# Kernel tuning notes

Measured on AMD Instinct MI355X. Metric: run time of the kernel, lower is better.

## Reference

```python
import jax, jax.numpy as jnp
import numpy as np
from jax import lax

B, S, F, H = 64, 512, 512, 1024
P = 0.5        # fixed power exponent (p_required_learn=False)
EPS = 1e-3     # epsilon default in forward


def setup_inputs() -> dict:
    key = jax.random.key(0)
    ks = jax.random.split(key, 10)
    x = jax.random.normal(ks[0], (B, S, F), dtype=jnp.float32)
    # monotonically nondecreasing times per batch row (arange fill)
    time_sequence = jnp.arange(B * S * 1, dtype=jnp.float32).reshape(B, S, 1)
    std = 1.0 / np.sqrt(H)
    def w(k, shape):
        return jax.random.normal(k, shape, dtype=jnp.float32) * std
    return {
        "x": x,
        "time_sequence": time_sequence,
        "U_r": w(ks[1], (F, H)), "W_r": w(ks[2], (H, H)),
        "b_r": jax.random.uniform(ks[3], (H,), jnp.float32, -std, std),
        "U_c": w(ks[4], (F, H)), "W_c": w(ks[5], (H, H)),
        "b_c": jax.random.uniform(ks[6], (H,), jnp.float32, -std, std),
        "U_o": w(ks[7], (F, H)), "W_o": w(ks[8], (H, H)),
        "b_o": jax.random.uniform(ks[9], (H,), jnp.float32, -std, std),
    }


def _plstm(x, time_sequence, U_r, W_r, b_r, U_c, W_c, b_c, U_o, W_o, b_o):
    b, s, f = x.shape
    h = W_r.shape[0]
    # input projections are h-independent: precompute for all timesteps
    xr = jnp.einsum('bsf,fh->bsh', x, U_r) + b_r  # [B,S,H]
    xc = jnp.einsum('bsf,fh->bsh', x, U_c) + b_c
    xo = jnp.einsum('bsf,fh->bsh', x, U_o) + b_o

    def step(carry, inp):
        h_t, c_t, k_t = carry
        xr_t, xc_t, xo_t, t = inp          # [B,H],[B,H],[B,H],[B,1]
        r_t = jax.nn.sigmoid(xr_t + h_t @ W_r)
        k_t = r_t * t + (1.0 - r_t) * k_t
        c_tilde = jnp.tanh(xc_t + h_t @ W_c)
        d = t - k_t
        f_t = ((d + 1.0) / (d + EPS)) ** (-P)
        c_t = f_t * c_t + (1.0 - f_t) * c_tilde
        o_t = jax.nn.sigmoid(xo_t + h_t @ W_o)
        h_t = o_t * jnp.tanh(c_t)
        return (h_t, c_t, k_t), h_t

    z = jnp.zeros((b, h), dtype=x.dtype)
    xs = (xr.transpose(1, 0, 2), xc.transpose(1, 0, 2), xo.transpose(1, 0, 2),
          time_sequence.transpose(1, 0, 2))
    (h_T, c_T, k_T), hs = lax.scan(step, (z, z, z), xs)
    hidden_seq = hs.transpose(1, 0, 2)  # [B,S,H]
    return hidden_seq, (h_T, c_T, k_T)


def reference(x, time_sequence, U_r, W_r, b_r, U_c, W_c, b_c, U_o, W_o, b_o):
    return _plstm(x, time_sequence, U_r, W_r, b_r, U_c, W_c, b_c, U_o, W_o, b_o)
```

## Files before the change

### kernel.cpp

```cpp
#include <hip/hip_runtime.h>
#include <hip/hip_fp16.h>
#include <cstdint>
#include <cstddef>

#define B_   64
#define S_   512
#define F_   512
#define H_   1024
#define KTOT 1536
#define EPS_ 1e-3f
#define NBLK 256
#define NTHR 512

typedef _Float16 f16x8 __attribute__((ext_vector_type(8)));
typedef float    f32x4 __attribute__((ext_vector_type(4)));

#define WS_CNT_OFF  0
#define WS_HBUF_OFF 4096
#define WS_WT_OFF   (1024*1024)

#define MFMA16(A,Bf,C) __builtin_amdgcn_mfma_f32_16x16x32_f16(A, Bf, C, 0, 0, 0)

__global__ void prep_weights(const float* __restrict__ Wr, const float* __restrict__ Wc,
                             const float* __restrict__ Wo, const float* __restrict__ Ur,
                             const float* __restrict__ Uc, const float* __restrict__ Uo,
                             _Float16* __restrict__ Wt) {
    int b  = blockIdx.x;
    int g  = b >> 6;
    int j0 = (b & 63) << 4;
    const float* W = (g == 0) ? Wr : (g == 1) ? Wc : Wo;
    const float* U = (g == 0) ? Ur : (g == 1) ? Uc : Uo;
    int jj = threadIdx.x & 15;
    int kk = threadIdx.x >> 4;
    for (int k0 = 0; k0 < KTOT; k0 += 16) {
        int k = k0 + kk;
        float v = (k < H_) ? W[(size_t)k * H_ + j0 + jj]
                           : U[(size_t)(k - H_) * H_ + j0 + jj];
        Wt[(size_t)(g * H_ + j0 + jj) * KTOT + k] = (_Float16)v;
    }
}

__global__ __launch_bounds__(NTHR, 2)
void plstm_cnt(const float* __restrict__ x,
               const float* __restrict__ ts,
               const float* __restrict__ br,
               const float* __restrict__ bc,
               const float* __restrict__ bo,
               const _Float16* __restrict__ Wt,
               _Float16* __restrict__ hbuf,
               unsigned* __restrict__ cnt,
               float* __restrict__ out) {
    __shared__ float    red[8 * 768];
    __shared__ _Float16 hlog[64 * 256];

    const int tid = threadIdx.x;
    const int bid = blockIdx.x;
    const int grp = bid >> 5;
    const int cg  = bid & 31;
    const int r0  = grp << 3;
    const int c0  = cg << 5;

    const int lane = tid & 63;
    const int w    = tid >> 6;
    const int arow = r0 + (lane & 7);
    const int kblk = lane >> 4;
    const int jcol = lane & 15;

    f16x8 bfh[3][2][4], bfx[3][2][2];
    #pragma unroll
    for (int g3 = 0; g3 < 3; ++g3)
        #pragma unroll
        for (int ct = 0; ct < 2; ++ct) {
            const _Float16* base = Wt + (size_t)(g3 * H_ + c0 + ct * 16 + jcol) * KTOT;
            #pragma unroll
            for (int sub = 0; sub < 4; ++sub)
                bfh[g3][ct][sub] = *(const f16x8*)(base + w * 128 + sub * 32 + kblk * 8);
            #pragma unroll
            for (int sub = 0; sub < 2; ++sub)
                bfx[g3][ct][sub] = *(const f16x8*)(base + H_ + w * 64 + sub * 32 + kblk * 8);
        }

    const int erow = tid >> 5;
    const int ecol = tid & 31;
    const int gb   = r0 + (erow & 7);
    const int gh   = c0 + ecol;
    float biasr = 0.f, biasc = 0.f, biaso = 0.f;
    if (tid < 256) { biasr = br[gh]; biasc = bc[gh]; biaso = bo[gh]; }
    float cst = 0.f, kst = 0.f, hval = 0.f;

    const unsigned* const cp = cnt + grp * 32;

    f32x4 xn0, xn1, xn2, xn3; float tvn = 0.f;
    {
        const float* xp = x + (size_t)arow * S_ * F_ + w * 64 + kblk * 8;
        xn0 = *(const f32x4*)xp;        xn1 = *(const f32x4*)(xp + 4);
        xn2 = *(const f32x4*)(xp + 32); xn3 = *(const f32x4*)(xp + 36);
        if (tid < 256) tvn = ts[(size_t)gb * S_];
        else if (w < 4) tvn = 0.f;
    }
    f16x8 xf0, xf1;
    #pragma unroll
    for (int r = 0; r < 4; ++r) { xf0[r] = (_Float16)xn0[r]; xf0[4 + r] = (_Float16)xn1[r]; }
    #pragma unroll
    for (int r = 0; r < 4; ++r) { xf1[r] = (_Float16)xn2[r]; xf1[4 + r] = (_Float16)xn3[r]; }
    float tv = tvn;

    for (int t = 0; t < S_; ++t) {
        f32x4 acc[3][2] = {};
        #pragma unroll
        for (int g3 = 0; g3 < 3; ++g3)
            #pragma unroll
            for (int ct = 0; ct < 2; ++ct) {
                acc[g3][ct] = MFMA16(xf0, bfx[g3][ct][0], acc[g3][ct]);
                acc[g3][ct] = MFMA16(xf1, bfx[g3][ct][1], acc[g3][ct]);
            }

        if (t > 0) {
            const unsigned tgt = 32u * (unsigned)t;
            unsigned c;
            for (unsigned it = 0; it < (1u << 17); ++it) {
                asm volatile("global_load_dword %0, %1, off sc0 sc1\n\t"
                             "s_waitcnt vmcnt(0)"
                             : "=v"(c) : "v"(cp) : "memory");
                if (c >= tgt) break;
            }
        }
        __builtin_amdgcn_sched_barrier(0);

        const _Float16* hb = hbuf + (size_t)(t % 3) * B_ * H_
                                  + (size_t)arow * H_ + w * 128 + kblk * 8;
        f16x8 hfr[4];
        #pragma unroll
        for (int s = 0; s < 4; ++s)
            asm volatile("global_load_dwordx4 %0, %1, off sc0 sc1"
                         : "=v"(hfr[s]) : "v"(hb + s * 32));
        asm volatile("s_waitcnt vmcnt(0)" ::: "memory");
        __builtin_amdgcn_sched_barrier(0);

        if (t + 1 < S_) {
            const float* xp = x + ((size_t)arow * S_ + (t + 1)) * F_ + w * 64 + kblk * 8;
            xn0 = *(const f32x4*)xp;        xn1 = *(const f32x4*)(xp + 4);
            xn2 = *(const f32x4*)(xp + 32); xn3 = *(const f32x4*)(xp + 36);
            if (tid < 256) tvn = ts[(size_t)gb * S_ + t + 1];
        }

        #pragma unroll
        for (int s = 0; s < 4; ++s)
            #pragma unroll
            for (int g3 = 0; g3 < 3; ++g3) {
                acc[g3][0] = MFMA16(hfr[s], bfh[g3][0][s], acc[g3][0]);
                acc[g3][1] = MFMA16(hfr[s], bfh[g3][1][s], acc[g3][1]);
            }

        if (lane < 32) {
            float* rw = red + w * 768;
            const int crow = (lane >> 4) << 2;
            const int ccol = lane & 15;
            #pragma unroll
            for (int i = 0; i < 4; ++i) {
                const int rr = (crow + i) * 32 + ccol;
                rw[rr]              = acc[0][0][i];  rw[rr + 16]         = acc[0][1][i];
                rw[256 + rr]        = acc[1][0][i];  rw[256 + rr + 16]   = acc[1][1][i];
                rw[512 + rr]        = acc[2][0][i];  rw[512 + rr + 16]   = acc[2][1][i];
            }
        }
        __syncthreads();

        float pr = biasr, pc = biasc, po = biaso;
        if (tid < 256) {
            #pragma unroll
            for (int ww = 0; ww < 8; ++ww) {
                pr += red[ww * 768 + tid];
                pc += red[ww * 768 + 256 + tid];
                po += red[ww * 768 + 512 + tid];
            }
        }

        if (tid < 256) {
            const float r = 1.f / (1.f + __expf(-pr));
            kst = r * tv + (1.f - r) * kst;
            const float e2 = __expf(2.f * pc);
            const float ctil = (e2 - 1.f) / (e2 + 1.f);
            const float d = tv - kst;
            const float f = __fsqrt_rn((d + EPS_) / (d + 1.f));
            cst = f * cst + (1.f - f) * ctil;
            const float o = 1.f / (1.f + __expf(-po));
            const float e2c = __expf(2.f * cst);
            hval = o * ((e2c - 1.f) / (e2c + 1.f));

            if (t + 1 < S_) {
                union { _Float16 hf; unsigned short us; } cv; cv.hf = (_Float16)hval;
                unsigned short* hp = (unsigned short*)(hbuf
                    + (size_t)((t + 1) % 3) * B_ * H_ + (size_t)gb * H_ + gh);
                unsigned uv = cv.us;
                asm volatile("global_store_short %0, %1, off sc0 sc1"
                             :: "v"(hp), "v"(uv) : "memory");
            }
            hlog[(t & 63) * 256 + tid] = (_Float16)hval;
        }

        asm volatile("s_waitcnt vmcnt(0)" ::: "memory");
        __syncthreads();
        if (tid == 0 && t + 1 < S_)
            __hip_atomic_fetch_add((unsigned*)cp, 1u,
                                   __ATOMIC_RELAXED, __HIP_MEMORY_SCOPE_AGENT);

        if (tid >= 256 && (t & 31) == 0 && t) {
            const int tbase = t - 32;
            #pragma unroll
            for (int p = 0; p < 4; ++p) {
                const int m  = p * 256 + (tid - 256);
                const int dt = m >> 5;
                const int c  = m & 31;
                f16x8 v = *(const f16x8*)(hlog + ((tbase + dt) & 63) * 256 + c * 8);
                float* op = out + ((size_t)(r0 + (c >> 2)) * S_ + tbase + dt) * H_
                                + c0 + (c & 3) * 8;
                f32x4 o0, o1;
                #pragma unroll
                for (int r2 = 0; r2 < 4; ++r2) { o0[r2] = (float)v[r2]; o1[r2] = (float)v[4 + r2]; }
                *(f32x4*)op = o0;
                *(f32x4*)(op + 4) = o1;
            }
        }

        if (t + 1 < S_) {
            #pragma unroll
            for (int r2 = 0; r2 < 4; ++r2) { xf0[r2] = (_Float16)xn0[r2]; xf0[4 + r2] = (_Float16)xn1[r2]; }
            #pragma unroll
            for (int r2 = 0; r2 < 4; ++r2) { xf1[r2] = (_Float16)xn2[r2]; xf1[4 + r2] = (_Float16)xn3[r2]; }
            tv = tvn;
        }
    }

    __syncthreads();
    {
        const int tbase = S_ - 32;
        #pragma unroll
        for (int p = 0; p < 2; ++p) {
            const int m  = p * 512 + tid;
            const int dt = m >> 5;
            const int c  = m & 31;
            f16x8 v = *(const f16x8*)(hlog + ((tbase + dt) & 63) * 256 + c * 8);
            float* op = out + ((size_t)(r0 + (c >> 2)) * S_ + tbase + dt) * H_
                            + c0 + (c & 3) * 8;
            f32x4 o0, o1;
            #pragma unroll
            for (int r2 = 0; r2 < 4; ++r2) { o0[r2] = (float)v[r2]; o1[r2] = (float)v[4 + r2]; }
            *(f32x4*)op = o0;
            *(f32x4*)(op + 4) = o1;
        }
    }
    if (tid < 256) {
        const size_t BSH = (size_t)B_ * S_ * H_;
        out[BSH +                       (size_t)gb * H_ + gh] = hval;
        out[BSH + (size_t)B_ * H_ +     (size_t)gb * H_ + gh] = cst;
        out[BSH + 2 * (size_t)B_ * H_ + (size_t)gb * H_ + gh] = kst;
    }
}

extern "C" void kernel_launch(void* const* d_in, const int* in_sizes, int n_in,
                              void* d_out, int out_size, void* d_ws, size_t ws_size,
                              hipStream_t stream) {
    (void)in_sizes; (void)n_in; (void)out_size; (void)ws_size;
    const float* x  = (const float*)d_in[0];
    const float* ts = (const float*)d_in[1];
    const float* Ur = (const float*)d_in[2];
    const float* Wr = (const float*)d_in[3];
    const float* br = (const float*)d_in[4];
    const float* Uc = (const float*)d_in[5];
    const float* Wc = (const float*)d_in[6];
    const float* bc = (const float*)d_in[7];
    const float* Uo = (const float*)d_in[8];
    const float* Wo = (const float*)d_in[9];
    const float* bo = (const float*)d_in[10];
    float* out = (float*)d_out;

    char* ws = (char*)d_ws;
    unsigned*  cnt  = (unsigned*)(ws + WS_CNT_OFF);
    _Float16*  hbuf = (_Float16*)(ws + WS_HBUF_OFF);
    _Float16*  Wt   = (_Float16*)(ws + WS_WT_OFF);

    hipMemsetAsync(ws, 0, WS_HBUF_OFF + 3 * B_ * H_ * 2, stream);

    prep_weights<<<192, 256, 0, stream>>>(Wr, Wc, Wo, Ur, Uc, Uo, Wt);

    plstm_cnt<<<NBLK, NTHR, 0, stream>>>(x, ts, br, bc, bo, Wt, hbuf, cnt, out);
}
```

Before: 1.813 ms.

## Pipeline spin-wait polling, stream hidden outputs per step, inflate LDS to force single occupancy

Replaces the serial spin-wait on the cross-block counter with two outstanding polling loads, so a fresh counter value arrives sooner after release. Batched hidden-state writeback every 32 steps is replaced by per-step scalar stores from the idle upper half of threads, removing the periodic write burst from the critical path. Shared memory moves to a 96KB dynamic allocation, which likely limits residency to one block per CU and so changes how the 256 persistent blocks map onto CUs. Per-step scalar stores are less coalesced than the earlier 32-byte vector stores.

```diff
diff --git a/kernel.cpp b/kernel.cpp
--- a/kernel.cpp
+++ b/kernel.cpp
@@ -18,6 +18,10 @@
 #define WS_CNT_OFF  0
 #define WS_HBUF_OFF 4096
 #define WS_WT_OFF   (1024*1024)
+
+#define LDS_RED   0
+#define LDS_HLOG  (24*1024)
+#define LDS_BYTES (96*1024)
 
 #define MFMA16(A,Bf,C) __builtin_amdgcn_mfma_f32_16x16x32_f16(A, Bf, C, 0, 0, 0)
 
@@ -50,8 +54,9 @@
                _Float16* __restrict__ hbuf,
                unsigned* __restrict__ cnt,
                float* __restrict__ out) {
-    __shared__ float    red[8 * 768];
-    __shared__ _Float16 hlog[64 * 256];
+    extern __shared__ char lds[];
+    float*    red  = (float*)(lds + LDS_RED);
+    _Float16* hlog = (_Float16*)(lds + LDS_HLOG);
 
     const int tid = threadIdx.x;
     const int bid = blockIdx.x;
@@ -96,7 +101,6 @@
         xn0 = *(const f32x4*)xp;        xn1 = *(const f32x4*)(xp + 4);
         xn2 = *(const f32x4*)(xp + 32); xn3 = *(const f32x4*)(xp + 36);
         if (tid < 256) tvn = ts[(size_t)gb * S_];
-        else if (w < 4) tvn = 0.f;
     }
     f16x8 xf0, xf1;
     #pragma unroll
@@ -117,15 +121,24 @@
 
         if (t > 0) {
             const unsigned tgt = 32u * (unsigned)t;
-            unsigned c;
-            for (unsigned it = 0; it < (1u << 17); ++it) {
-                asm volatile("global_load_dword %0, %1, off sc0 sc1\n\t"
-                             "s_waitcnt vmcnt(0)"
-                             : "=v"(c) : "v"(cp) : "memory");
-                if (c >= tgt) break;
-            }
-        }
-        __builtin_amdgcn_sched_barrier(0);
+            asm volatile("s_waitcnt vmcnt(0)" ::: "memory");
+            __builtin_amdgcn_sched_barrier(0);
+            unsigned ca, cb;
+            asm volatile("global_load_dword %0, %1, off sc0 sc1" : "=v"(ca) : "v"(cp));
+            asm volatile("global_load_dword %0, %1, off sc0 sc1" : "=v"(cb) : "v"(cp));
+            for (unsigned it = 0; it < (1u << 16); ++it) {
+                asm volatile("s_waitcnt vmcnt(1)" ::: "memory");
+                __builtin_amdgcn_sched_barrier(0);
+                if (ca >= tgt) break;
+                asm volatile("global_load_dword %0, %1, off sc0 sc1" : "=v"(ca) : "v"(cp));
+                asm volatile("s_waitcnt vmcnt(1)" ::: "memory");
+                __builtin_amdgcn_sched_barrier(0);
+                if (cb >= tgt) break;
+                asm volatile("global_load_dword %0, %1, off sc0 sc1" : "=v"(cb) : "v"(cp));
+            }
+            asm volatile("s_waitcnt vmcnt(0)" ::: "memory");
+            __builtin_amdgcn_sched_barrier(0);
+        }
 
         const _Float16* hb = hbuf + (size_t)(t % 3) * B_ * H_
                                   + (size_t)arow * H_ + w * 128 + kblk * 8;
@@ -196,7 +209,7 @@
                 asm volatile("global_store_short %0, %1, off sc0 sc1"
                              :: "v"(hp), "v"(uv) : "memory");
             }
-            hlog[(t & 63) * 256 + tid] = (_Float16)hval;
+            hlog[(t & 3) * 256 + tid] = (_Float16)hval;
         }
 
         asm volatile("s_waitcnt vmcnt(0)" ::: "memory");
@@ -205,22 +218,10 @@
             __hip_atomic_fetch_add((unsigned*)cp, 1u,
                                    __ATOMIC_RELAXED, __HIP_MEMORY_SCOPE_AGENT);
 
-        if (tid >= 256 && (t & 31) == 0 && t) {
-            const int tbase = t - 32;
-            #pragma unroll
-            for (int p = 0; p < 4; ++p) {
-                const int m  = p * 256 + (tid - 256);
-                const int dt = m >> 5;
-                const int c  = m & 31;
-                f16x8 v = *(const f16x8*)(hlog + ((tbase + dt) & 63) * 256 + c * 8);
-                float* op = out + ((size_t)(r0 + (c >> 2)) * S_ + tbase + dt) * H_
-                                + c0 + (c & 3) * 8;
-                f32x4 o0, o1;
-                #pragma unroll
-                for (int r2 = 0; r2 < 4; ++r2) { o0[r2] = (float)v[r2]; o1[r2] = (float)v[4 + r2]; }
-                *(f32x4*)op = o0;
-                *(f32x4*)(op + 4) = o1;
-            }
+        if (tid >= 256 && t > 0) {
+            const int m = tid - 256;
+            const float hv = (float)hlog[((t - 1) & 3) * 256 + m];
+            out[((size_t)(r0 + (m >> 5)) * S_ + (t - 1)) * H_ + c0 + (m & 31)] = hv;
         }
 
         if (t + 1 < S_) {
@@ -233,22 +234,10 @@
     }
 
     __syncthreads();
-    {
-        const int tbase = S_ - 32;
-        #pragma unroll
-        for (int p = 0; p < 2; ++p) {
-            const int m  = p * 512 + tid;
-            const int dt = m >> 5;
-            const int c  = m & 31;
-            f16x8 v = *(const f16x8*)(hlog + ((tbase + dt) & 63) * 256 + c * 8);
-            float* op = out + ((size_t)(r0 + (c >> 2)) * S_ + tbase + dt) * H_
-                            + c0 + (c & 3) * 8;
-            f32x4 o0, o1;
-            #pragma unroll
-            for (int r2 = 0; r2 < 4; ++r2) { o0[r2] = (float)v[r2]; o1[r2] = (float)v[4 + r2]; }
-            *(f32x4*)op = o0;
-            *(f32x4*)(op + 4) = o1;
-        }
+    if (tid >= 256) {
+        const int m = tid - 256;
+        const float hv = (float)hlog[((S_ - 1) & 3) * 256 + m];
+        out[((size_t)(r0 + (m >> 5)) * S_ + (S_ - 1)) * H_ + c0 + (m & 31)] = hv;
     }
     if (tid < 256) {
         const size_t BSH = (size_t)B_ * S_ * H_;
@@ -284,5 +273,7 @@
 
     prep_weights<<<192, 256, 0, stream>>>(Wr, Wc, Wo, Ur, Uc, Uo, Wt);
 
-    plstm_cnt<<<NBLK, NTHR, 0, stream>>>(x, ts, br, bc, bo, Wt, hbuf, cnt, out);
+    hipFuncSetAttribute((const void*)plstm_cnt,
+                        hipFuncAttributeMaxDynamicSharedMemorySize, LDS_BYTES);
+    plstm_cnt<<<NBLK, NTHR, LDS_BYTES, stream>>>(x, ts, br, bc, bo, Wt, hbuf, cnt, out);
 }
```

Result: slower. 1.933 ms (+6.6%).
